# Performance work log

Hardware: AMD Instinct MI355X
Metric: run time of the kernel (lower is better)

The kernel has to match this reference:

```python
import jax, jax.numpy as jnp
import numpy as np

D_VOC, P_VOC, M_VOC = 2048, 1024, 4096
H = 256
T = 32
LD, LP, LM = 24, 12, 20


def _norm_adj(key, n):
    # binary graph + self loops, row-normalized (matches GCN.normalize(adj+I))
    a = (jax.random.uniform(key, (n, n)) < 0.002).astype(jnp.float32)
    a = a + jnp.eye(n, dtype=jnp.float32)
    rs = a.sum(axis=1)
    rinv = jnp.where(rs > 0, 1.0 / rs, 0.0)
    return rinv[:, None] * a


def setup_inputs() -> dict:
    key = jax.random.key(0)
    ks = jax.random.split(key, 32)
    s = float(1.0 / np.sqrt(H))
    u = lambda k, shape, sc: jax.random.uniform(k, shape, minval=-sc, maxval=sc, dtype=jnp.float32)
    inp = {
        'diag_codes': jax.random.randint(ks[0], (T, LD), 0, D_VOC),
        'proc_codes': jax.random.randint(ks[1], (T, LP), 0, P_VOC),
        'med_codes': jax.random.randint(ks[2], (T - 1, LM), 0, M_VOC),
        'diag_emb': u(ks[3], (D_VOC, H), 0.1),
        'proc_emb': u(ks[4], (P_VOC, H), 0.1),
        'gru_d_wih': u(ks[5], (3 * H, H), s), 'gru_d_whh': u(ks[6], (3 * H, H), s),
        'gru_d_bih': u(ks[7], (3 * H,), s), 'gru_d_bhh': u(ks[8], (3 * H,), s),
        'gru_p_wih': u(ks[9], (3 * H, H), s), 'gru_p_whh': u(ks[10], (3 * H, H), s),
        'gru_p_bih': u(ks[11], (3 * H,), s), 'gru_p_bhh': u(ks[12], (3 * H,), s),
        'q_w': u(ks[13], (2 * H, H), s), 'q_b': u(ks[14], (H,), s),
        'adj_ehr': _norm_adj(ks[15], M_VOC),
        'adj_ddi': _norm_adj(ks[16], M_VOC),
        'w1_ehr': u(ks[17], (M_VOC, H), s), 'b1_ehr': u(ks[18], (H,), s),
        'w2_ehr': u(ks[19], (H, H), s), 'b2_ehr': u(ks[20], (H,), s),
        'w1_ddi': u(ks[21], (M_VOC, H), s), 'b1_ddi': u(ks[22], (H,), s),
        'w2_ddi': u(ks[23], (H, H), s), 'b2_ddi': u(ks[24], (H,), s),
        'inter': jax.random.normal(ks[25], (1,), dtype=jnp.float32) / H,
        'proj_w': u(ks[26], (2 * H, H), s), 'proj_b': u(ks[27], (H,), s),
    }
    return inp


def _gru(x, wih, whh, bih, bhh):
    # torch.nn.GRU cell math; x: [T, H] -> outputs [T, H]
    def step(h, xt):
        gi = xt @ wih.T + bih
        gh = h @ whh.T + bhh
        ir, iz, inn = jnp.split(gi, 3)
        hr, hz, hn = jnp.split(gh, 3)
        r = jax.nn.sigmoid(ir + hr)
        z = jax.nn.sigmoid(iz + hz)
        n = jnp.tanh(inn + r * hn)
        h2 = (1.0 - z) * n + z * h
        return h2, h2
    _, ys = jax.lax.scan(step, jnp.zeros((x.shape[-1],), x.dtype), x)
    return ys


def _gcn(adj, w1, b1, w2, b2):
    # input features are identity, so first support mm(I, w1) == w1
    h1 = jax.nn.relu(adj @ w1 + b1)
    return adj @ (h1 @ w2) + b2


def reference(diag_codes, proc_codes, med_codes, diag_emb, proc_emb,
              gru_d_wih, gru_d_whh, gru_d_bih, gru_d_bhh,
              gru_p_wih, gru_p_whh, gru_p_bih, gru_p_bhh,
              q_w, q_b, adj_ehr, adj_ddi,
              w1_ehr, b1_ehr, w2_ehr, b2_ehr,
              w1_ddi, b1_ddi, w2_ddi, b2_ddi,
              inter, proj_w, proj_b):
    # ---- PatientEncoder: gather + sum codes per visit, GRU over visits ----
    seq_d = diag_emb[diag_codes].sum(axis=1)            # [T, H]
    seq_p = proc_emb[proc_codes].sum(axis=1)            # [T, H]
    od = _gru(seq_d, gru_d_wih, gru_d_whh, gru_d_bih, gru_d_bhh)
    op = _gru(seq_p, gru_p_wih, gru_p_whh, gru_p_bih, gru_p_bhh)
    feats = jnp.concatenate([od, op], axis=-1)          # [T, 2H]
    queries = jax.nn.relu(feats) @ q_w + q_b            # [T, H] (Sequential(ReLU, Linear))
    query = queries[-1:]                                # [1, H]
    history_keys = queries[:-1]                         # [T-1, H]
    # multi-hot history medication values (scatter)
    tm1 = med_codes.shape[0]
    history_values = jnp.zeros((tm1, M_VOC), jnp.float32).at[
        jnp.arange(tm1)[:, None], med_codes].set(1.0)   # [T-1, M_VOC]
    # ---- PriorEncoder ----
    prior = _gcn(adj_ehr, w1_ehr, b1_ehr, w2_ehr, b2_ehr) \
        - inter[0] * _gcn(adj_ddi, w1_ddi, b1_ddi, w2_ddi, b2_ddi)  # [M_VOC, H]
    w_emb = jax.nn.softmax(query @ prior.T, axis=-1)    # [1, M_VOC]
    # diag(w) @ prior == broadcast row-scale (the fused gather-weighted-scale)
    gc1 = w_emb.reshape(-1, 1) * prior                  # [M_VOC, H]
    visit_w = jax.nn.softmax(query @ history_keys.T, axis=-1)  # [1, T-1]
    wv = (visit_w @ history_values).reshape(-1, 1)      # [M_VOC, 1]
    gc2 = wv * prior                                    # [M_VOC, H]
    return jnp.concatenate([gc1, gc2], axis=-1) @ proj_w + proj_b  # [M_VOC, H]
```

## Files before the change

kernel.cpp:

```cpp
#include <hip/hip_runtime.h>
#include <hip/hip_bf16.h>

#define HD   256
#define TT   32
#define MV   4096
#define LD_  24
#define LP_  12
#define LM_  20
#define MAXNZ 96

typedef _Float16 h2v __attribute__((ext_vector_type(2)));
typedef _Float16 h8  __attribute__((ext_vector_type(8)));

__device__ __forceinline__ float fdot2(h2v a, h2v b, float c) {
#if __has_builtin(__builtin_amdgcn_fdot2)
  return __builtin_amdgcn_fdot2(a, b, c, false);
#else
  return c + (float)a[0] * (float)b[0] + (float)a[1] * (float)b[1];
#endif
}

__global__ __launch_bounds__(768) void k0_cvt(
    const float* __restrict__ whh_d, const float* __restrict__ whh_p,
    h8* __restrict__ wt)
{
  const int i = blockIdx.x, b = blockIdx.y, g = threadIdx.x;
  const float* whh = b ? whh_p : whh_d;
  const float* src = whh + (size_t)g * HD + 8 * i;
  h8 v;
#pragma unroll
  for (int e = 0; e < 8; ++e) v[e] = (_Float16)src[e];
  wt[((size_t)b * 32 + i) * 768 + g] = v;
}

__global__ __launch_bounds__(768) void k1_embed_gi(
    const int* __restrict__ dc, const int* __restrict__ pc,
    const float* __restrict__ demb, const float* __restrict__ pemb,
    const float* __restrict__ wih_d, const float* __restrict__ bih_d,
    const float* __restrict__ wih_p, const float* __restrict__ bih_p,
    float* __restrict__ GI)
{
  const int t = blockIdx.x, b = blockIdx.y;
  const int* codes = b ? pc : dc;
  const int L = b ? LP_ : LD_;
  const float* emb = b ? pemb : demb;
  const float* wih = b ? wih_p : wih_d;
  const float* bih = b ? bih_p : bih_d;
  __shared__ float s[HD];
  const int j = threadIdx.x;
  if (j < HD) {
    float acc = 0.f;
    for (int l = 0; l < L; ++l) acc += emb[(size_t)codes[t * L + l] * HD + j];
    s[j] = acc;
  }
  __syncthreads();
  const int g = j;
  float acc = bih[g];
  const float* wr = wih + (size_t)g * HD;
  for (int k = 0; k < HD; k += 4) {
    float4 w4 = *(const float4*)(wr + k);
    acc = fmaf(w4.x, s[k], acc);
    acc = fmaf(w4.y, s[k + 1], acc);
    acc = fmaf(w4.z, s[k + 2], acc);
    acc = fmaf(w4.w, s[k + 3], acc);
  }
  GI[((size_t)b * TT + t) * 768 + g] = acc;
}

__global__ __launch_bounds__(768, 3) void k2_gru(
    const float* __restrict__ GI, const h8* __restrict__ wt,
    const float* __restrict__ bhh_d, const float* __restrict__ bhh_p,
    float* __restrict__ feats)
{
  const int b = blockIdx.x, g = threadIdx.x;
  const float* gi = GI + (size_t)b * TT * 768;
  const float* bhh = b ? bhh_p : bhh_d;

  __shared__ float GIs[TT * 768];
  __shared__ h8 hh8[32];
  __shared__ float ghs[768];

  {
    const float4* s4 = (const float4*)gi;
    float4* d4 = (float4*)GIs;
#pragma unroll
    for (int i = 0; i < 8; ++i) d4[g + 768 * i] = s4[g + 768 * i];
  }

  h2v w[128];
  {
    const h8* wrow = wt + (size_t)b * 32 * 768 + g;
#pragma unroll
    for (int i = 0; i < 32; ++i) {
      union { h8 v; h2v p[4]; } u;
      u.v = wrow[(size_t)i * 768];
      w[4 * i + 0] = u.p[0];
      w[4 * i + 1] = u.p[1];
      w[4 * i + 2] = u.p[2];
      w[4 * i + 3] = u.p[3];
    }
  }
#pragma unroll
  for (int i = 0; i < 128; ++i) {
    float tmp = __builtin_bit_cast(float, w[i]);
    asm volatile("" : "+v"(tmp));
    w[i] = __builtin_bit_cast(h2v, tmp);
  }

  const float bh = bhh[g];
  float hreg = 0.f;
  if (g < HD) ((_Float16*)hh8)[g] = (_Float16)0.f;
  __syncthreads();

  for (int t = 0; t < TT; ++t) {
    float d0 = 0.f, d1 = 0.f, d2 = 0.f, d3 = 0.f;
#pragma unroll
    for (int i = 0; i < 32; ++i) {
      union { h8 v; h2v p[4]; } u;
      u.v = hh8[i];
      d0 = fdot2(w[4 * i + 0], u.p[0], d0);
      d1 = fdot2(w[4 * i + 1], u.p[1], d1);
      d2 = fdot2(w[4 * i + 2], u.p[2], d2);
      d3 = fdot2(w[4 * i + 3], u.p[3], d3);
    }
    ghs[g] = (d0 + d1) + (d2 + d3) + bh;
    __syncthreads();
    if (g < HD) {
      const float* git = GIs + t * 768;
      float ir = git[g], iz = git[HD + g], inn = git[2 * HD + g];
      float hr = ghs[g], hz = ghs[HD + g], hn = ghs[2 * HD + g];
      float r = 1.f / (1.f + __expf(-(ir + hr)));
      float z = 1.f / (1.f + __expf(-(iz + hz)));
      float n = tanhf(inn + r * hn);
      hreg = (1.f - z) * n + z * hreg;
      ((_Float16*)hh8)[g] = (_Float16)hreg;
      feats[(size_t)t * 512 + b * HD + g] = hreg;
    }
    __syncthreads();
  }
}

__global__ __launch_bounds__(256) void k2b_queries(
    const float* __restrict__ feats, const float* __restrict__ q_w,
    const float* __restrict__ q_b, float* __restrict__ queries)
{
  const int t = blockIdx.x, j = threadIdx.x;
  __shared__ float f[512];
  f[j] = fmaxf(feats[(size_t)t * 512 + j], 0.f);
  f[j + 256] = fmaxf(feats[(size_t)t * 512 + 256 + j], 0.f);
  __syncthreads();
  float acc = q_b[j];
  for (int k = 0; k < 512; ++k) acc = fmaf(f[k], q_w[(size_t)k * HD + j], acc);
  queries[(size_t)t * HD + j] = acc;
}

__global__ __launch_bounds__(256) void k3_scan(
    const float* __restrict__ adj_e, const float* __restrict__ adj_d,
    const float* __restrict__ w1_e, const float* __restrict__ b1_e,
    const float* __restrict__ w1_d, const float* __restrict__ b1_d,
    float* __restrict__ h1, int* __restrict__ cnt_g,
    int* __restrict__ cols_g, float* __restrict__ vals_g)
{
  const int r = blockIdx.x, b = blockIdx.y, j = threadIdx.x;
  const float* adj = (b ? adj_d : adj_e) + (size_t)r * MV;
  const float* w1 = b ? w1_d : w1_e;
  const float* b1 = b ? b1_d : b1_e;

  __shared__ int pA[256], pB[256];
  __shared__ int scols[MAXNZ];
  __shared__ float svals[MAXNZ];

  const float4* row4 = (const float4*)adj;
  float4 v0 = row4[0 * 256 + j];
  float4 v1 = row4[1 * 256 + j];
  float4 v2 = row4[2 * 256 + j];
  float4 v3 = row4[3 * 256 + j];
  int cl = 0;
  cl += (v0.x != 0.f) + (v0.y != 0.f) + (v0.z != 0.f) + (v0.w != 0.f);
  cl += (v1.x != 0.f) + (v1.y != 0.f) + (v1.z != 0.f) + (v1.w != 0.f);
  cl += (v2.x != 0.f) + (v2.y != 0.f) + (v2.z != 0.f) + (v2.w != 0.f);
  cl += (v3.x != 0.f) + (v3.y != 0.f) + (v3.z != 0.f) + (v3.w != 0.f);

  pA[j] = cl;
  __syncthreads();
  int* src = pA; int* dst = pB;
  for (int ofs = 1; ofs < 256; ofs <<= 1) {
    dst[j] = src[j] + (j >= ofs ? src[j - ofs] : 0);
    __syncthreads();
    int* tmp = src; src = dst; dst = tmp;
  }
  const int total = src[255];
  int pos = src[j] - cl;

#define EMIT(VV, CI, CE)                                        \
  { float val = (VV);                                           \
    if (val != 0.f) { if (pos < MAXNZ) { scols[pos] = (CI) * 1024 + 4 * j + (CE); svals[pos] = val; } ++pos; } }
  EMIT(v0.x, 0, 0) EMIT(v0.y, 0, 1) EMIT(v0.z, 0, 2) EMIT(v0.w, 0, 3)
  EMIT(v1.x, 1, 0) EMIT(v1.y, 1, 1) EMIT(v1.z, 1, 2) EMIT(v1.w, 1, 3)
  EMIT(v2.x, 2, 0) EMIT(v2.y, 2, 1) EMIT(v2.z, 2, 2) EMIT(v2.w, 2, 3)
  EMIT(v3.x, 3, 0) EMIT(v3.y, 3, 1) EMIT(v3.z, 3, 2) EMIT(v3.w, 3, 3)
#undef EMIT
  __syncthreads();

  const int n = total > MAXNZ ? MAXNZ : total;
  float acc = b1[j];
  for (int k = 0; k < n; ++k)
    acc = fmaf(svals[k], w1[(size_t)scols[k] * HD + j], acc);

  const size_t rowg = (size_t)b * MV + r;
  h1[rowg * HD + j] = fmaxf(acc, 0.f);
  if (j == 0) cnt_g[rowg] = n;
  if (j < n) {
    cols_g[rowg * MAXNZ + j] = scols[j];
    vals_g[rowg * MAXNZ + j] = svals[j];
  }
}

__global__ __launch_bounds__(512) void k4_z(
    const float* __restrict__ h1, const float* __restrict__ w2_e,
    const float* __restrict__ w2_d, float* __restrict__ zz)
{
  const int blk = blockIdx.x, b = blockIdx.y;
  const int t = threadIdx.x;
  const int j = t & 255, half = t >> 8;
  const float* w2 = b ? w2_d : w2_e;
  const float* h1b = h1 + (size_t)b * MV * HD + (size_t)blk * 8 * HD;
  __shared__ float tile[8][HD];
  __shared__ float part[8][HD];
  {
    float4* t4 = (float4*)tile;
    const float4* s4 = (const float4*)h1b;
    t4[t] = s4[t];
  }
  __syncthreads();
  float acc[8];
#pragma unroll
  for (int r = 0; r < 8; ++r) acc[r] = 0.f;
  const int k0 = half * 128;
  for (int k = k0; k < k0 + 128; k += 4) {
    float wa = w2[(size_t)(k + 0) * HD + j];
    float wb = w2[(size_t)(k + 1) * HD + j];
    float wc = w2[(size_t)(k + 2) * HD + j];
    float wd = w2[(size_t)(k + 3) * HD + j];
#pragma unroll
    for (int r = 0; r < 8; ++r) {
      float4 tv = *(const float4*)&tile[r][k];
      acc[r] = fmaf(tv.x, wa, acc[r]);
      acc[r] = fmaf(tv.y, wb, acc[r]);
      acc[r] = fmaf(tv.z, wc, acc[r]);
      acc[r] = fmaf(tv.w, wd, acc[r]);
    }
  }
  if (half == 1) {
#pragma unroll
    for (int r = 0; r < 8; ++r) part[r][j] = acc[r];
  }
  __syncthreads();
  if (half == 0) {
    float* zb = zz + (size_t)b * MV * HD + (size_t)blk * 8 * HD;
#pragma unroll
    for (int r = 0; r < 8; ++r) zb[r * HD + j] = acc[r] + part[r][j];
  }
}

__global__ __launch_bounds__(256) void k5_prior(
    const float* __restrict__ zz, const int* __restrict__ cnt_g,
    const int* __restrict__ cols_g, const float* __restrict__ vals_g,
    const float* __restrict__ b2_e, const float* __restrict__ b2_d,
    const float* __restrict__ inter, const float* __restrict__ queries,
    float* __restrict__ prior, float* __restrict__ s1)
{
  const int r = blockIdx.x, j = threadIdx.x;
  __shared__ float red[256];
  float acc_e = b2_e[j];
  {
    const int ne = cnt_g[r];
    const int* ce = cols_g + (size_t)r * MAXNZ;
    const float* ve = vals_g + (size_t)r * MAXNZ;
    for (int k = 0; k < ne; ++k)
      acc_e = fmaf(ve[k], zz[(size_t)ce[k] * HD + j], acc_e);
  }
  float acc_d = b2_d[j];
  {
    const int nd = cnt_g[MV + r];
    const int* cd = cols_g + (size_t)(MV + r) * MAXNZ;
    const float* vd = vals_g + (size_t)(MV + r) * MAXNZ;
    const float* zd = zz + (size_t)MV * HD;
    for (int k = 0; k < nd; ++k)
      acc_d = fmaf(vd[k], zd[(size_t)cd[k] * HD + j], acc_d);
  }
  const float pr = acc_e - inter[0] * acc_d;
  prior[(size_t)r * HD + j] = pr;
  red[j] = queries[31 * HD + j] * pr;
  __syncthreads();
  for (int s = 128; s > 0; s >>= 1) {
    if (j < s) red[j] += red[j + s];
    __syncthreads();
  }
  if (j == 0) s1[r] = red[0];
}

__global__ __launch_bounds__(1024) void k6a_softmax(
    const float* __restrict__ s1, const float* __restrict__ queries,
    float* __restrict__ w_emb, float* __restrict__ visw)
{
  const int j = threadIdx.x;
  __shared__ float red[1024];
  __shared__ float s2[31];
  float m = -1e30f;
  for (int i = j; i < MV; i += 1024) m = fmaxf(m, s1[i]);
  red[j] = m;
  __syncthreads();
  for (int s = 512; s > 0; s >>= 1) {
    if (j < s) red[j] = fmaxf(red[j], red[j + s]);
    __syncthreads();
  }
  const float mx = red[0];
  __syncthreads();
  float sum = 0.f;
  for (int i = j; i < MV; i += 1024) sum += __expf(s1[i] - mx);
  red[j] = sum;
  __syncthreads();
  for (int s = 512; s > 0; s >>= 1) {
    if (j < s) red[j] += red[j + s];
    __syncthreads();
  }
  const float inv = 1.f / red[0];
  for (int i = j; i < MV; i += 1024) w_emb[i] = __expf(s1[i] - mx) * inv;

  if (j < 31) {
    float acc = 0.f;
    for (int k = 0; k < HD; ++k)
      acc = fmaf(queries[31 * HD + k], queries[(size_t)j * HD + k], acc);
    s2[j] = acc;
  }
  __syncthreads();
  if (j == 0) {
    float mm = -1e30f;
    for (int t = 0; t < 31; ++t) mm = fmaxf(mm, s2[t]);
    float ss = 0.f;
    for (int t = 0; t < 31; ++t) ss += __expf(s2[t] - mm);
    const float is = 1.f / ss;
    for (int t = 0; t < 31; ++t) visw[t] = __expf(s2[t] - mm) * is;
  }
}

__global__ __launch_bounds__(1024) void k6b_wv(
    const int* __restrict__ med, const float* __restrict__ visw,
    float* __restrict__ wv)
{
  __shared__ int mc[31 * LM_];
  __shared__ float vw[31];
  const int j = threadIdx.x;
  if (j < 31 * LM_) mc[j] = med[j];
  if (j < 31) vw[j] = visw[j];
  __syncthreads();
  const int m = blockIdx.x * 1024 + j;
  float acc = 0.f;
  for (int t = 0; t < 31; ++t) {
    bool found = false;
#pragma unroll
    for (int l = 0; l < LM_; ++l) found = found || (mc[t * LM_ + l] == m);
    if (found) acc += vw[t];
  }
  wv[m] = acc;
}

__global__ __launch_bounds__(512) void k7_out(
    const float* __restrict__ prior, const float* __restrict__ w_emb,
    const float* __restrict__ wv, const float* __restrict__ proj_w,
    const float* __restrict__ proj_b, float* __restrict__ out)
{
  const int blk = blockIdx.x;
  const int t = threadIdx.x;
  const int j = t & 255, half = t >> 8;
  const int r0 = blk * 8;
  __shared__ float tile[8][HD];
  __shared__ float part[8][HD];
  __shared__ float we[8], wvv[8];
  {
    float4* t4 = (float4*)tile;
    const float4* s4 = (const float4*)(prior + (size_t)r0 * HD);
    t4[t] = s4[t];
  }
  if (t < 8) { we[t] = w_emb[r0 + t]; wvv[t] = wv[r0 + t]; }
  __syncthreads();
  const float* wmat = proj_w + (size_t)half * HD * HD;
  float acc[8];
#pragma unroll
  for (int r = 0; r < 8; ++r) acc[r] = 0.f;
  for (int k = 0; k < HD; k += 4) {
    float wa = wmat[(size_t)(k + 0) * HD + j];
    float wb = wmat[(size_t)(k + 1) * HD + j];
    float wc = wmat[(size_t)(k + 2) * HD + j];
    float wd = wmat[(size_t)(k + 3) * HD + j];
#pragma unroll
    for (int r = 0; r < 8; ++r) {
      float4 tv = *(const float4*)&tile[r][k];
      acc[r] = fmaf(tv.x, wa, acc[r]);
      acc[r] = fmaf(tv.y, wb, acc[r]);
      acc[r] = fmaf(tv.z, wc, acc[r]);
      acc[r] = fmaf(tv.w, wd, acc[r]);
    }
  }
  if (half == 1) {
#pragma unroll
    for (int r = 0; r < 8; ++r) part[r][j] = acc[r];
  }
  __syncthreads();
  if (half == 0) {
    const float pb = proj_b[j];
#pragma unroll
    for (int r = 0; r < 8; ++r)
      out[(size_t)(r0 + r) * HD + j] = we[r] * acc[r] + wvv[r] * part[r][j] + pb;
  }
}

extern "C" void kernel_launch(void* const* d_in, const int* in_sizes, int n_in,
                              void* d_out, int out_size, void* d_ws, size_t ws_size,
                              hipStream_t stream) {
  const int* diag_codes = (const int*)d_in[0];
  const int* proc_codes = (const int*)d_in[1];
  const int* med_codes  = (const int*)d_in[2];
  const float* diag_emb = (const float*)d_in[3];
  const float* proc_emb = (const float*)d_in[4];
  const float* wih_d = (const float*)d_in[5];
  const float* whh_d = (const float*)d_in[6];
  const float* bih_d = (const float*)d_in[7];
  const float* bhh_d = (const float*)d_in[8];
  const float* wih_p = (const float*)d_in[9];
  const float* whh_p = (const float*)d_in[10];
  const float* bih_p = (const float*)d_in[11];
  const float* bhh_p = (const float*)d_in[12];
  const float* q_w = (const float*)d_in[13];
  const float* q_b = (const float*)d_in[14];
  const float* adj_ehr = (const float*)d_in[15];
  const float* adj_ddi = (const float*)d_in[16];
  const float* w1_ehr = (const float*)d_in[17];
  const float* b1_ehr = (const float*)d_in[18];
  const float* w2_ehr = (const float*)d_in[19];
  const float* b2_ehr = (const float*)d_in[20];
  const float* w1_ddi = (const float*)d_in[21];
  const float* b1_ddi = (const float*)d_in[22];
  const float* w2_ddi = (const float*)d_in[23];
  const float* b2_ddi = (const float*)d_in[24];
  const float* inter = (const float*)d_in[25];
  const float* proj_w = (const float*)d_in[26];
  const float* proj_b = (const float*)d_in[27];
  float* out = (float*)d_out;

  float* ws = (float*)d_ws;
  size_t off = 0;
  float* GI      = ws + off; off += 2 * TT * 768;
  float* feats   = ws + off; off += TT * 512;
  float* queries = ws + off; off += TT * HD;
  float* h1      = ws + off; off += 2 * (size_t)MV * HD;
  float* zz      = ws + off; off += 2 * (size_t)MV * HD;
  float* prior   = ws + off; off += (size_t)MV * HD;
  float* s1      = ws + off; off += MV;
  float* w_emb   = ws + off; off += MV;
  float* visw    = ws + off; off += 32;
  float* wv      = ws + off; off += MV;
  int*   cnt_g   = (int*)(ws + off); off += 2 * MV;
  int*   cols_g  = (int*)(ws + off); off += 2 * (size_t)MV * MAXNZ;
  float* vals_g  = ws + off; off += 2 * (size_t)MV * MAXNZ;
  h8*    wt      = (h8*)(ws + off); off += 2 * 32 * 768 * 4;
  (void)ws_size; (void)in_sizes; (void)n_in; (void)out_size;

  k0_cvt<<<dim3(32, 2), 768, 0, stream>>>(whh_d, whh_p, wt);
  k1_embed_gi<<<dim3(TT, 2), 768, 0, stream>>>(diag_codes, proc_codes, diag_emb,
      proc_emb, wih_d, bih_d, wih_p, bih_p, GI);
  k2_gru<<<2, 768, 0, stream>>>(GI, wt, bhh_d, bhh_p, feats);
  k2b_queries<<<TT, 256, 0, stream>>>(feats, q_w, q_b, queries);
  k3_scan<<<dim3(MV, 2), 256, 0, stream>>>(adj_ehr, adj_ddi, w1_ehr, b1_ehr,
      w1_ddi, b1_ddi, h1, cnt_g, cols_g, vals_g);
  k4_z<<<dim3(MV / 8, 2), 512, 0, stream>>>(h1, w2_ehr, w2_ddi, zz);
  k5_prior<<<MV, 256, 0, stream>>>(zz, cnt_g, cols_g, vals_g, b2_ehr, b2_ddi,
      inter, queries, prior, s1);
  k6a_softmax<<<1, 1024, 0, stream>>>(s1, queries, w_emb, visw);
  k6b_wv<<<MV / 1024, 1024, 0, stream>>>(med_codes, visw, wv);
  k7_out<<<MV / 8, 512, 0, stream>>>(prior, w_emb, wv, proj_w, proj_b, out);
}
```

Measured before the change: 227.4 us.

## Restructure GRU to one thread per hidden unit and warp-per-row adjacency scan

The GRU kernel now runs 256 threads, each holding all three gate weight rows in registers (384 packed half2 values). This removes the shared-memory gate exchange and one barrier per step, and double-buffers the hidden state. The adjacency scan maps one 64-lane wavefront per row, using shuffle-based prefix sums and float4 gathers of w1 in place of block-wide shared-memory scans. That scan is also launched before the GRU in stream order. Holding that many weight registers per thread risks spills or very low occupancy, and the GRU now reads GI directly from global memory each step.

```diff
diff --git a/kernel.cpp b/kernel.cpp
--- a/kernel.cpp
+++ b/kernel.cpp
@@ -19,6 +19,10 @@
   return c + (float)a[0] * (float)b[0] + (float)a[1] * (float)b[1];
 #endif
 }
+
+#define PIN2(x) { float _t = __builtin_bit_cast(float, x); \
+                  asm volatile("" : "+v"(_t));             \
+                  x = __builtin_bit_cast(h2v, _t); }
 
 __global__ __launch_bounds__(768) void k0_cvt(
     const float* __restrict__ whh_d, const float* __restrict__ whh_p,
@@ -67,7 +71,9 @@
   GI[((size_t)b * TT + t) * 768 + g] = acc;
 }
 
-__global__ __launch_bounds__(768, 3) void k2_gru(
+__global__ __launch_bounds__(256)
+__attribute__((amdgpu_waves_per_eu(1, 1)))
+void k2_gru(
     const float* __restrict__ GI, const h8* __restrict__ wt,
     const float* __restrict__ bhh_d, const float* __restrict__ bhh_p,
     float* __restrict__ feats)
@@ -76,66 +82,65 @@
   const float* gi = GI + (size_t)b * TT * 768;
   const float* bhh = b ? bhh_p : bhh_d;
 
-  __shared__ float GIs[TT * 768];
-  __shared__ h8 hh8[32];
-  __shared__ float ghs[768];
-
+  __shared__ h8 hbuf[2][32];
+
+  h2v wr_[128], wz_[128], wn_[128];
   {
-    const float4* s4 = (const float4*)gi;
-    float4* d4 = (float4*)GIs;
-#pragma unroll
-    for (int i = 0; i < 8; ++i) d4[g + 768 * i] = s4[g + 768 * i];
-  }
-
-  h2v w[128];
-  {
-    const h8* wrow = wt + (size_t)b * 32 * 768 + g;
+    const h8* wbase = wt + (size_t)b * 32 * 768;
 #pragma unroll
     for (int i = 0; i < 32; ++i) {
       union { h8 v; h2v p[4]; } u;
-      u.v = wrow[(size_t)i * 768];
-      w[4 * i + 0] = u.p[0];
-      w[4 * i + 1] = u.p[1];
-      w[4 * i + 2] = u.p[2];
-      w[4 * i + 3] = u.p[3];
+      u.v = wbase[(size_t)i * 768 + g];
+      wr_[4*i+0] = u.p[0]; wr_[4*i+1] = u.p[1];
+      wr_[4*i+2] = u.p[2]; wr_[4*i+3] = u.p[3];
+      u.v = wbase[(size_t)i * 768 + 256 + g];
+      wz_[4*i+0] = u.p[0]; wz_[4*i+1] = u.p[1];
+      wz_[4*i+2] = u.p[2]; wz_[4*i+3] = u.p[3];
+      u.v = wbase[(size_t)i * 768 + 512 + g];
+      wn_[4*i+0] = u.p[0]; wn_[4*i+1] = u.p[1];
+      wn_[4*i+2] = u.p[2]; wn_[4*i+3] = u.p[3];
     }
   }
 #pragma unroll
-  for (int i = 0; i < 128; ++i) {
-    float tmp = __builtin_bit_cast(float, w[i]);
-    asm volatile("" : "+v"(tmp));
-    w[i] = __builtin_bit_cast(h2v, tmp);
-  }
-
-  const float bh = bhh[g];
+  for (int i = 0; i < 128; ++i) { PIN2(wr_[i]) PIN2(wz_[i]) PIN2(wn_[i]) }
+
+  const float bh_r = bhh[g], bh_z = bhh[256 + g], bh_n = bhh[512 + g];
   float hreg = 0.f;
-  if (g < HD) ((_Float16*)hh8)[g] = (_Float16)0.f;
+  ((_Float16*)&hbuf[0][0])[g] = (_Float16)0.f;
   __syncthreads();
 
   for (int t = 0; t < TT; ++t) {
-    float d0 = 0.f, d1 = 0.f, d2 = 0.f, d3 = 0.f;
+    const float* git = gi + t * 768;
+    float ir = git[g], iz = git[256 + g], inn = git[512 + g];
+
+    const h8* hb = hbuf[t & 1];
+    float ar0 = 0.f, ar1 = 0.f, az0 = 0.f, az1 = 0.f, an0 = 0.f, an1 = 0.f;
 #pragma unroll
     for (int i = 0; i < 32; ++i) {
       union { h8 v; h2v p[4]; } u;
-      u.v = hh8[i];
-      d0 = fdot2(w[4 * i + 0], u.p[0], d0);
-      d1 = fdot2(w[4 * i + 1], u.p[1], d1);
-      d2 = fdot2(w[4 * i + 2], u.p[2], d2);
-      d3 = fdot2(w[4 * i + 3], u.p[3], d3);
+      u.v = hb[i];
+      ar0 = fdot2(wr_[4*i+0], u.p[0], ar0);
+      ar1 = fdot2(wr_[4*i+1], u.p[1], ar1);
+      ar0 = fdot2(wr_[4*i+2], u.p[2], ar0);
+      ar1 = fdot2(wr_[4*i+3], u.p[3], ar1);
+      az0 = fdot2(wz_[4*i+0], u.p[0], az0);
+      az1 = fdot2(wz_[4*i+1], u.p[1], az1);
+      az0 = fdot2(wz_[4*i+2], u.p[2], az0);
+      az1 = fdot2(wz_[4*i+3], u.p[3], az1);
+      an0 = fdot2(wn_[4*i+0], u.p[0], an0);
+      an1 = fdot2(wn_[4*i+1], u.p[1], an1);
+      an0 = fdot2(wn_[4*i+2], u.p[2], an0);
+      an1 = fdot2(wn_[4*i+3], u.p[3], an1);
     }
-    ghs[g] = (d0 + d1) + (d2 + d3) + bh;
-    __syncthreads();
-    if (g < HD) {
-      const float* git = GIs + t * 768;
-      float ir = git[g], iz = git[HD + g], inn = git[2 * HD + g];
-      float hr = ghs[g], hz = ghs[HD + g], hn = ghs[2 * HD + g];
-      float r = 1.f / (1.f + __expf(-(ir + hr)));
-      float z = 1.f / (1.f + __expf(-(iz + hz)));
-      float n = tanhf(inn + r * hn);
-      hreg = (1.f - z) * n + z * hreg;
-      ((_Float16*)hh8)[g] = (_Float16)hreg;
-      feats[(size_t)t * 512 + b * HD + g] = hreg;
-    }
+    const float hr = ar0 + ar1 + bh_r;
+    const float hz = az0 + az1 + bh_z;
+    const float hn = an0 + an1 + bh_n;
+    const float r = 1.f / (1.f + __expf(-(ir + hr)));
+    const float z = 1.f / (1.f + __expf(-(iz + hz)));
+    const float n = tanhf(inn + r * hn);
+    hreg = (1.f - z) * n + z * hreg;
+    ((_Float16*)&hbuf[(t & 1) ^ 1][0])[g] = (_Float16)hreg;
+    feats[(size_t)t * 512 + b * HD + g] = hreg;
     __syncthreads();
   }
 }
@@ -154,65 +159,78 @@
   queries[(size_t)t * HD + j] = acc;
 }
 
-__global__ __launch_bounds__(256) void k3_scan(
+__global__ __launch_bounds__(512) void k3_scan(
     const float* __restrict__ adj_e, const float* __restrict__ adj_d,
     const float* __restrict__ w1_e, const float* __restrict__ b1_e,
     const float* __restrict__ w1_d, const float* __restrict__ b1_d,
     float* __restrict__ h1, int* __restrict__ cnt_g,
     int* __restrict__ cols_g, float* __restrict__ vals_g)
 {
-  const int r = blockIdx.x, b = blockIdx.y, j = threadIdx.x;
-  const float* adj = (b ? adj_d : adj_e) + (size_t)r * MV;
-  const float* w1 = b ? w1_d : w1_e;
-  const float* b1 = b ? b1_d : b1_e;
-
-  __shared__ int pA[256], pB[256];
-  __shared__ int scols[MAXNZ];
-  __shared__ float svals[MAXNZ];
-
-  const float4* row4 = (const float4*)adj;
-  float4 v0 = row4[0 * 256 + j];
-  float4 v1 = row4[1 * 256 + j];
-  float4 v2 = row4[2 * 256 + j];
-  float4 v3 = row4[3 * 256 + j];
+  const int w = threadIdx.x >> 6, lane = threadIdx.x & 63;
+  const int rg = blockIdx.x * 8 + w;
+  const int bsel = rg >> 12;
+  const int r = rg & (MV - 1);
+  const float* adj = (bsel ? adj_d : adj_e) + (size_t)r * MV;
+  const float* w1 = bsel ? w1_d : w1_e;
+  const float* b1 = bsel ? b1_d : b1_e;
+
+  __shared__ int   scols[8][MAXNZ];
+  __shared__ float svals[8][MAXNZ];
+
+  float4 ev[16];
+#pragma unroll
+  for (int c = 0; c < 16; ++c)
+    ev[c] = *(const float4*)(adj + c * 256 + lane * 4);
+
   int cl = 0;
-  cl += (v0.x != 0.f) + (v0.y != 0.f) + (v0.z != 0.f) + (v0.w != 0.f);
-  cl += (v1.x != 0.f) + (v1.y != 0.f) + (v1.z != 0.f) + (v1.w != 0.f);
-  cl += (v2.x != 0.f) + (v2.y != 0.f) + (v2.z != 0.f) + (v2.w != 0.f);
-  cl += (v3.x != 0.f) + (v3.y != 0.f) + (v3.z != 0.f) + (v3.w != 0.f);
-
-  pA[j] = cl;
-  __syncthreads();
-  int* src = pA; int* dst = pB;
-  for (int ofs = 1; ofs < 256; ofs <<= 1) {
-    dst[j] = src[j] + (j >= ofs ? src[j - ofs] : 0);
-    __syncthreads();
-    int* tmp = src; src = dst; dst = tmp;
-  }
-  const int total = src[255];
-  int pos = src[j] - cl;
-
-#define EMIT(VV, CI, CE)                                        \
-  { float val = (VV);                                           \
-    if (val != 0.f) { if (pos < MAXNZ) { scols[pos] = (CI) * 1024 + 4 * j + (CE); svals[pos] = val; } ++pos; } }
-  EMIT(v0.x, 0, 0) EMIT(v0.y, 0, 1) EMIT(v0.z, 0, 2) EMIT(v0.w, 0, 3)
-  EMIT(v1.x, 1, 0) EMIT(v1.y, 1, 1) EMIT(v1.z, 1, 2) EMIT(v1.w, 1, 3)
-  EMIT(v2.x, 2, 0) EMIT(v2.y, 2, 1) EMIT(v2.z, 2, 2) EMIT(v2.w, 2, 3)
-  EMIT(v3.x, 3, 0) EMIT(v3.y, 3, 1) EMIT(v3.z, 3, 2) EMIT(v3.w, 3, 3)
-#undef EMIT
-  __syncthreads();
-
+#pragma unroll
+  for (int c = 0; c < 16; ++c)
+    cl += (ev[c].x != 0.f) + (ev[c].y != 0.f) + (ev[c].z != 0.f) + (ev[c].w != 0.f);
+
+  int pref = cl;
+#pragma unroll
+  for (int ofs = 1; ofs < 64; ofs <<= 1) {
+    int v = __shfl_up(pref, ofs, 64);
+    if (lane >= ofs) pref += v;
+  }
+  const int total = __shfl(pref, 63, 64);
+  int pos = pref - cl;
+
+#pragma unroll
+  for (int c = 0; c < 16; ++c) {
+    const float vv[4] = {ev[c].x, ev[c].y, ev[c].z, ev[c].w};
+#pragma unroll
+    for (int e = 0; e < 4; ++e) {
+      if (vv[e] != 0.f) {
+        if (pos < MAXNZ) {
+          scols[w][pos] = c * 256 + lane * 4 + e;
+          svals[w][pos] = vv[e];
+        }
+        ++pos;
+      }
+    }
+  }
   const int n = total > MAXNZ ? MAXNZ : total;
-  float acc = b1[j];
-  for (int k = 0; k < n; ++k)
-    acc = fmaf(svals[k], w1[(size_t)scols[k] * HD + j], acc);
-
-  const size_t rowg = (size_t)b * MV + r;
-  h1[rowg * HD + j] = fmaxf(acc, 0.f);
-  if (j == 0) cnt_g[rowg] = n;
-  if (j < n) {
-    cols_g[rowg * MAXNZ + j] = scols[j];
-    vals_g[rowg * MAXNZ + j] = svals[j];
+
+  float4 acc = *(const float4*)(b1 + lane * 4);
+  for (int k = 0; k < n; ++k) {
+    const int col = scols[w][k];
+    const float v = svals[w][k];
+    const float4 wv4 = *(const float4*)(w1 + (size_t)col * HD + lane * 4);
+    acc.x = fmaf(v, wv4.x, acc.x);
+    acc.y = fmaf(v, wv4.y, acc.y);
+    acc.z = fmaf(v, wv4.z, acc.z);
+    acc.w = fmaf(v, wv4.w, acc.w);
+  }
+  float4 hro;
+  hro.x = fmaxf(acc.x, 0.f); hro.y = fmaxf(acc.y, 0.f);
+  hro.z = fmaxf(acc.z, 0.f); hro.w = fmaxf(acc.w, 0.f);
+  *(float4*)(h1 + (size_t)rg * HD + lane * 4) = hro;
+
+  if (lane == 0) cnt_g[rg] = n;
+  for (int k = lane; k < n; k += 64) {
+    cols_g[(size_t)rg * MAXNZ + k] = scols[w][k];
+    vals_g[(size_t)rg * MAXNZ + k] = svals[w][k];
   }
 }
 
@@ -470,10 +488,10 @@
   k0_cvt<<<dim3(32, 2), 768, 0, stream>>>(whh_d, whh_p, wt);
   k1_embed_gi<<<dim3(TT, 2), 768, 0, stream>>>(diag_codes, proc_codes, diag_emb,
       proc_emb, wih_d, bih_d, wih_p, bih_p, GI);
-  k2_gru<<<2, 768, 0, stream>>>(GI, wt, bhh_d, bhh_p, feats);
+  k3_scan<<<2 * MV / 8, 512, 0, stream>>>(adj_ehr, adj_ddi, w1_ehr, b1_ehr,
+      w1_ddi, b1_ddi, h1, cnt_g, cols_g, vals_g);
+  k2_gru<<<2, 256, 0, stream>>>(GI, wt, bhh_d, bhh_p, feats);
   k2b_queries<<<TT, 256, 0, stream>>>(feats, q_w, q_b, queries);
-  k3_scan<<<dim3(MV, 2), 256, 0, stream>>>(adj_ehr, adj_ddi, w1_ehr, b1_ehr,
-      w1_ddi, b1_ddi, h1, cnt_g, cols_g, vals_g);
   k4_z<<<dim3(MV / 8, 2), 512, 0, stream>>>(h1, w2_ehr, w2_ddi, zz);
   k5_prior<<<MV, 256, 0, stream>>>(zz, cnt_g, cols_g, vals_g, b2_ehr, b2_ddi,
       inter, queries, prior, s1);
```

Measured after the change: 257.9 us. 13.4% more time.
